# Kernel tuning notes

Measured on AMD Instinct MI355X. Metric: run time of the kernel, lower is better.

Reference implementation:

```python
import jax, jax.numpy as jnp
import numpy as np

S, M, E = 8192, 4096, 64          # tokens, model_dim, num_experts
CAPACITY_FACTOR = 1.0
MIN_CAPACITY = 8
CAPACITY = max(int(np.ceil(S / E * CAPACITY_FACTOR)), MIN_CAPACITY)  # 128


def setup_inputs() -> dict:
    key = jax.random.key(0)
    k1, k2 = jax.random.split(key)
    x = jax.random.normal(k1, (S, M), dtype=jnp.float32)
    wg = jax.random.normal(k2, (E, M), dtype=jnp.float32) * (1.0 / np.sqrt(M))
    return {"x": x, "wg": wg}


def reference(x, wg):
    # gate projection (Linear, no bias): logits [s, e]
    logits = jnp.einsum('sm,em->se', x, wg)
    gates = jax.nn.softmax(logits, axis=1)                      # [s, e]

    # top-1 expert per token
    indices1_s = jnp.argmax(gates, axis=1)                      # [s]
    mask1 = jax.nn.one_hot(indices1_s, E, dtype=jnp.int32)      # [s, e]
    exp_counts = jnp.sum(mask1, axis=0)                         # [e]

    # load-balancing aux loss
    me = jnp.mean(gates, axis=0)
    ce = jnp.mean(mask1.astype(jnp.float32), axis=0)
    l_aux = jnp.sum(me * ce) * E

    # capacity drop (use_rts=False): keep first CAPACITY tokens per expert.
    # torch: top_idx = topk(mask1, capacity, dim=0)[1]; scatter ones at those rows.
    top_idx = jax.lax.top_k(mask1.T, CAPACITY)[1]               # [e, c] token ids
    keep = jnp.zeros((S, E), dtype=jnp.int32).at[top_idx.T, jnp.arange(E)[None, :]].set(1)
    mask1 = mask1 * keep                                        # [s, e]

    # position of each token inside its expert's buffer
    locations1 = jnp.cumsum(mask1, axis=0) - 1                  # [s, e]
    locations1_s = jnp.sum(locations1 * mask1, axis=1)          # [s]

    mask1_f = mask1.astype(gates.dtype)
    gates_masked = gates * mask1_f                              # [s, e]
    locations1_sc = jax.nn.one_hot(locations1_s, CAPACITY, dtype=jnp.float32)  # [s, c]

    combine_weights = jnp.einsum('se,sc->sec', gates_masked, locations1_sc)    # [s, e, c]
    dispatch_mask = combine_weights.astype(bool)
    return l_aux, combine_weights, dispatch_mask, exp_counts
```

## Files before the change

### kernel.cpp

```cpp
#include <hip/hip_runtime.h>
#include <hip/hip_bf16.h>

#define TS 8192
#define TM 4096
#define TE 64
#define TCAP 128
static const size_t CW = (size_t)TS * TE * TCAP;
static const size_t OUT_ELEMS = 1 + 2 * CW + TE;
static const size_t OUT_BYTES = OUT_ELEMS * sizeof(float);

#define BM 128
#define BK 16
#define SA 132
#define SW 68

__global__ __launch_bounds__(256) void gemm_partial(
    const float* __restrict__ x, const float* __restrict__ wg,
    float* __restrict__ part, int kchunk) {
  __shared__ float As[BK][SA];
  __shared__ float Ws[BK][SW];
  const int tid = threadIdx.x;
  const int t0 = blockIdx.x * BM;
  const int k0 = blockIdx.y * kchunk;
  const int ntile = kchunk / BK;
  const int tg = tid >> 3;
  const int eg = tid & 7;

  float acc[4][8] = {};
  float4 ra[2]; float4 rw;

  auto load_tile = [&](int kt) {
    const int kb = k0 + kt * BK;
#pragma unroll
    for (int i = 0; i < 2; i++) {
      int idx = tid + 256 * i;
      int tok = idx >> 2, c4 = idx & 3;
      ra[i] = *(const float4*)&x[(size_t)(t0 + tok) * TM + kb + 4 * c4];
    }
    int e = tid >> 2, c4 = tid & 3;
    rw = *(const float4*)&wg[(size_t)e * TM + kb + 4 * c4];
  };

  load_tile(0);
  for (int kt = 0; kt < ntile; kt++) {
#pragma unroll
    for (int i = 0; i < 2; i++) {
      int idx = tid + 256 * i;
      int tok = idx >> 2, c4 = idx & 3;
      As[4 * c4 + 0][tok] = ra[i].x; As[4 * c4 + 1][tok] = ra[i].y;
      As[4 * c4 + 2][tok] = ra[i].z; As[4 * c4 + 3][tok] = ra[i].w;
    }
    { int e = tid >> 2, c4 = tid & 3;
      Ws[4 * c4 + 0][e] = rw.x; Ws[4 * c4 + 1][e] = rw.y;
      Ws[4 * c4 + 2][e] = rw.z; Ws[4 * c4 + 3][e] = rw.w; }
    __syncthreads();
    if (kt + 1 < ntile) load_tile(kt + 1);
#pragma unroll
    for (int k = 0; k < BK; k++) {
      float4 a0 = *(const float4*)&As[k][tg * 4];
      float4 b0 = *(const float4*)&Ws[k][eg * 8];
      float4 b1 = *(const float4*)&Ws[k][eg * 8 + 4];
      float av[4] = {a0.x, a0.y, a0.z, a0.w};
      float bv[8] = {b0.x, b0.y, b0.z, b0.w, b1.x, b1.y, b1.z, b1.w};
#pragma unroll
      for (int i = 0; i < 4; i++)
#pragma unroll
        for (int j = 0; j < 8; j++) acc[i][j] += av[i] * bv[j];
    }
    __syncthreads();
  }
  float* dst = part + (size_t)blockIdx.y * TS * TE;
#pragma unroll
  for (int i = 0; i < 4; i++) {
    int tok = t0 + tg * 4 + i;
#pragma unroll
    for (int j = 0; j < 8; j += 4) {
      float4 v = make_float4(acc[i][j], acc[i][j + 1], acc[i][j + 2], acc[i][j + 3]);
      *(float4*)&dst[(size_t)tok * TE + eg * 8 + j] = v;
    }
  }
}

__global__ __launch_bounds__(256) void softmax_top1(
    const float* __restrict__ part, int KS,
    float* __restrict__ gates, float* __restrict__ gate1, int* __restrict__ idx1) {
  const int s = blockIdx.x * 4 + (threadIdx.x >> 6);
  const int lane = threadIdx.x & 63;
  float logit = 0.0f;
  for (int p = 0; p < KS; p++)
    logit += part[((size_t)p * TS + s) * TE + lane];

  float mv = logit; int mi = lane;
#pragma unroll
  for (int off = 32; off; off >>= 1) {
    float ov = __shfl_xor(mv, off);
    int oi = __shfl_xor(mi, off);
    if (ov > mv || (ov == mv && oi < mi)) { mv = ov; mi = oi; }
  }
  float ex = expf(logit - mv);
  float sum = ex;
#pragma unroll
  for (int off = 32; off; off >>= 1) sum += __shfl_xor(sum, off);
  float g = ex / sum;
  gates[(size_t)s * TE + lane] = g;
  if (lane == mi) { gate1[s] = g; idx1[s] = mi; }
}

__global__ __launch_bounds__(256) void stats(
    const float* __restrict__ gates, const int* __restrict__ idx1,
    float* __restrict__ me, int* __restrict__ pos, int* __restrict__ counts) {
  const int e = blockIdx.x, tid = threadIdx.x;
  float s = 0.0f;
  for (int t = tid; t < TS; t += 256) s += gates[(size_t)t * TE + e];
  __shared__ float red[256];
  red[tid] = s; __syncthreads();
  for (int o = 128; o; o >>= 1) { if (tid < o) red[tid] += red[tid + o]; __syncthreads(); }
  if (tid == 0) me[e] = red[0];

  if (tid < 64) {
    const int lane = tid;
    int base = 0;
    for (int c = 0; c < TS / 64; c++) {
      int sTok = c * 64 + lane;
      bool m = (idx1[sTok] == e);
      unsigned long long mask = __ballot(m);
      if (m) {
        int p = base + __popcll(mask & ((1ull << lane) - 1ull));
        pos[sTok] = (p < TCAP) ? p : -1;
      }
      base += __popcll(mask);
    }
    if (lane == 0) counts[e] = base;
  }
}

__global__ __launch_bounds__(256) void scatter_out(
    const float* __restrict__ gate1, const int* __restrict__ idx1,
    const int* __restrict__ pos, const float* __restrict__ me,
    const int* __restrict__ counts, float* __restrict__ out, size_t cw) {
  if (blockIdx.x == TS / 256) {
    const int lane = threadIdx.x;
    if (lane < 64) {
      float v = (me[lane] / (float)TS) * ((float)counts[lane] / (float)TS);
      float sum = v;
#pragma unroll
      for (int off = 32; off; off >>= 1) sum += __shfl_xor(sum, off);
      if (lane == 0) out[0] = sum * (float)TE;
      out[1 + 2 * cw + lane] = (float)counts[lane];
    }
    return;
  }
  const int s = blockIdx.x * 256 + threadIdx.x;
  int p = pos[s];
  if (p >= 0) {
    size_t off = 1 + ((size_t)s * TE + idx1[s]) * (size_t)TCAP + (size_t)p;
    out[off] = gate1[s];
    out[off + cw] = 1.0f;
  }
}

extern "C" void kernel_launch(void* const* d_in, const int* in_sizes, int n_in,
                              void* d_out, int out_size, void* d_ws, size_t ws_size,
                              hipStream_t stream) {
  const float* x = (const float*)d_in[0];
  const float* wg = (const float*)d_in[1];
  float* out = (float*)d_out;

  const size_t SE = (size_t)TS * TE;
  int KS = 8;
  auto need = [&](int ks) {
    return (size_t)ks * SE * 4 + SE * 4 + (size_t)TS * 12 + 1024;
  };
  while (KS > 1 && need(KS) > ws_size) KS >>= 1;

  float* part  = (float*)d_ws;
  float* gates = part + (size_t)KS * SE;
  float* gate1 = gates + SE;
  int*   idx1  = (int*)(gate1 + TS);
  int*   pos   = idx1 + TS;
  float* me    = (float*)(pos + TS);
  int*   cnts  = (int*)(me + TE);

  hipMemsetAsync(d_out, 0, OUT_BYTES, stream);

  dim3 ggrid(TS / BM, KS);
  gemm_partial<<<ggrid, 256, 0, stream>>>(x, wg, part, TM / KS);
  softmax_top1<<<TS / 4, 256, 0, stream>>>(part, KS, gates, gate1, idx1);
  stats<<<TE, 256, 0, stream>>>(gates, idx1, me, pos, cnts);
  scatter_out<<<TS / 256 + 1, 256, 0, stream>>>(gate1, idx1, pos, me, cnts, out, CW);
}
```

Baseline: 684.2 us.

## Fuse output zeroing into GEMM launch and scatter directly from stats

Replaces the separate hipMemsetAsync of the huge output (about 268M floats, roughly 1 GB) with extra blocks in the GEMM kernel that write zeros using nontemporal vector stores. The zeroing can then overlap with the gate GEMM. The per-expert stats kernel now writes the combine and dispatch entries directly, which removes the pos buffer and the separate scatter kernel. The l_aux and counts finalisation moves to a tiny kernel. The risk is that zero blocks compete with GEMM blocks for bandwidth, and that the zeroing has no ordering guarantee against the later scatter beyond kernel boundaries.

```diff
diff --git a/kernel.cpp b/kernel.cpp
--- a/kernel.cpp
+++ b/kernel.cpp
@@ -5,23 +5,37 @@
 #define TM 4096
 #define TE 64
 #define TCAP 128
-static const size_t CW = (size_t)TS * TE * TCAP;
-static const size_t OUT_ELEMS = 1 + 2 * CW + TE;
-static const size_t OUT_BYTES = OUT_ELEMS * sizeof(float);
+static constexpr size_t CW = (size_t)TS * TE * TCAP;
+static constexpr size_t OUT_ELEMS = 1 + 2 * CW + TE;
+static constexpr size_t NF4 = (OUT_ELEMS - 1) / 4;
+
+typedef float v4f __attribute__((ext_vector_type(4)));
 
 #define BM 128
 #define BK 16
 #define SA 132
 #define SW 68
+#define ZB 1024
 
-__global__ __launch_bounds__(256) void gemm_partial(
+__global__ __launch_bounds__(256) void gemm_zero(
     const float* __restrict__ x, const float* __restrict__ wg,
-    float* __restrict__ part, int kchunk) {
+    float* __restrict__ part, float* __restrict__ out, int kchunk, int nGemm) {
+  if ((int)blockIdx.x >= nGemm) {
+    const int zb = blockIdx.x - nGemm;
+    const v4f z = {0.f, 0.f, 0.f, 0.f};
+    v4f* o4 = (v4f*)out;
+    const size_t stride = (size_t)ZB * 256;
+    for (size_t i = (size_t)zb * 256 + threadIdx.x; i < NF4; i += stride)
+      __builtin_nontemporal_store(z, &o4[i]);
+    return;
+  }
   __shared__ float As[BK][SA];
   __shared__ float Ws[BK][SW];
   const int tid = threadIdx.x;
-  const int t0 = blockIdx.x * BM;
-  const int k0 = blockIdx.y * kchunk;
+  const int bx = blockIdx.x % (TS / BM);
+  const int ky = blockIdx.x / (TS / BM);
+  const int t0 = bx * BM;
+  const int k0 = ky * kchunk;
   const int ntile = kchunk / BK;
   const int tg = tid >> 3;
   const int eg = tid & 7;
@@ -69,7 +83,7 @@
     }
     __syncthreads();
   }
-  float* dst = part + (size_t)blockIdx.y * TS * TE;
+  float* dst = part + (size_t)ky * TS * TE;
 #pragma unroll
   for (int i = 0; i < 4; i++) {
     int tok = t0 + tg * 4 + i;
@@ -106,9 +120,10 @@
   if (lane == mi) { gate1[s] = g; idx1[s] = mi; }
 }
 
-__global__ __launch_bounds__(256) void stats(
+__global__ __launch_bounds__(256) void stats_scatter(
     const float* __restrict__ gates, const int* __restrict__ idx1,
-    float* __restrict__ me, int* __restrict__ pos, int* __restrict__ counts) {
+    const float* __restrict__ gate1, float* __restrict__ me,
+    int* __restrict__ counts, float* __restrict__ out) {
   const int e = blockIdx.x, tid = threadIdx.x;
   float s = 0.0f;
   for (int t = tid; t < TS; t += 256) s += gates[(size_t)t * TE + e];
@@ -126,7 +141,11 @@
       unsigned long long mask = __ballot(m);
       if (m) {
         int p = base + __popcll(mask & ((1ull << lane) - 1ull));
-        pos[sTok] = (p < TCAP) ? p : -1;
+        if (p < TCAP) {
+          size_t off = 1 + ((size_t)sTok * TE + e) * (size_t)TCAP + (size_t)p;
+          out[off] = gate1[sTok];
+          out[off + CW] = 1.0f;
+        }
       }
       base += __popcll(mask);
     }
@@ -134,29 +153,15 @@
   }
 }
 
-__global__ __launch_bounds__(256) void scatter_out(
-    const float* __restrict__ gate1, const int* __restrict__ idx1,
-    const int* __restrict__ pos, const float* __restrict__ me,
-    const int* __restrict__ counts, float* __restrict__ out, size_t cw) {
-  if (blockIdx.x == TS / 256) {
-    const int lane = threadIdx.x;
-    if (lane < 64) {
-      float v = (me[lane] / (float)TS) * ((float)counts[lane] / (float)TS);
-      float sum = v;
+__global__ void finalize_laux(const float* __restrict__ me, const int* __restrict__ counts,
+                              float* __restrict__ out) {
+  const int lane = threadIdx.x;
+  float v = (me[lane] / (float)TS) * ((float)counts[lane] / (float)TS);
+  float sum = v;
 #pragma unroll
-      for (int off = 32; off; off >>= 1) sum += __shfl_xor(sum, off);
-      if (lane == 0) out[0] = sum * (float)TE;
-      out[1 + 2 * cw + lane] = (float)counts[lane];
-    }
-    return;
-  }
-  const int s = blockIdx.x * 256 + threadIdx.x;
-  int p = pos[s];
-  if (p >= 0) {
-    size_t off = 1 + ((size_t)s * TE + idx1[s]) * (size_t)TCAP + (size_t)p;
-    out[off] = gate1[s];
-    out[off + cw] = 1.0f;
-  }
+  for (int off = 32; off; off >>= 1) sum += __shfl_xor(sum, off);
+  if (lane == 0) out[0] = sum * (float)TE;
+  out[1 + 2 * CW + lane] = (float)counts[lane];
 }
 
 extern "C" void kernel_launch(void* const* d_in, const int* in_sizes, int n_in,
@@ -177,15 +182,12 @@
   float* gates = part + (size_t)KS * SE;
   float* gate1 = gates + SE;
   int*   idx1  = (int*)(gate1 + TS);
-  int*   pos   = idx1 + TS;
-  float* me    = (float*)(pos + TS);
+  float* me    = (float*)(idx1 + TS);
   int*   cnts  = (int*)(me + TE);
 
-  hipMemsetAsync(d_out, 0, OUT_BYTES, stream);
-
-  dim3 ggrid(TS / BM, KS);
-  gemm_partial<<<ggrid, 256, 0, stream>>>(x, wg, part, TM / KS);
+  const int nGemm = (TS / BM) * KS;
+  gemm_zero<<<nGemm + ZB, 256, 0, stream>>>(x, wg, part, out, TM / KS, nGemm);
   softmax_top1<<<TS / 4, 256, 0, stream>>>(part, KS, gates, gate1, idx1);
-  stats<<<TE, 256, 0, stream>>>(gates, idx1, me, pos, cnts);
-  scatter_out<<<TS / 256 + 1, 256, 0, stream>>>(gate1, idx1, pos, me, cnts, out, CW);
+  stats_scatter<<<TE, 256, 0, stream>>>(gates, idx1, gate1, me, cnts, out);
+  finalize_laux<<<1, 64, 0, stream>>>(me, cnts, out);
 }
```

After: 704.7 us. +3.0%, slower.
